# Performance work log

Measured on AMD Instinct MI355X. Metric: run time of the kernel, lower is better.

The kernel has to match this reference:

```python
import jax, jax.numpy as jnp
import numpy as np

B, N, T, E = 8, 512, 2048, 4096
D, TD, L = 768, 128, 4
V, TYPES = 30522, 64
MAX_NODE_LEN = 512


def setup_inputs() -> dict:
    key = jax.random.key(0)
    ks = jax.random.split(key, 12)
    tok_per_node = T // N  # 4 tokens per node
    node_types = jax.random.randint(ks[0], (B, N), 0, TYPES)
    node_token_ids = jax.random.randint(ks[1], (B, T), 0, V)
    token_seg_ids = jnp.tile(jnp.arange(T, dtype=jnp.int32) // tok_per_node, (B, 1))
    node_token_lens = jnp.full((B, N), tok_per_node, dtype=jnp.int32)
    graph_node_lens = jnp.full((B,), N, dtype=jnp.int32)
    edge_src = jax.random.randint(ks[2], (B, E), 0, N)
    edge_dst = jax.random.randint(ks[3], (B, E), 0, N)
    # edges_attrs used as PyG edge_weight (original passes LongTensor); cast to float
    edge_weight = jax.random.randint(ks[4], (B, E), 1, 4).astype(jnp.float32)
    s = 0.02
    type_table = jax.random.normal(ks[5], (TYPES, TD)) * s
    word_emb = jax.random.normal(ks[6], (V, D)) * s
    fusion_w = jax.random.normal(ks[7], (TD + D, D)) * s
    fusion_b = jnp.zeros((D,), jnp.float32)
    ggnn_w = jax.random.normal(ks[8], (L, D, D)) * s  # per-layer message weight
    gru_w_ih = jax.random.normal(ks[9], (3 * D, D)) * s  # [W_ir; W_iz; W_in]
    gru_w_hh = jax.random.normal(ks[10], (3 * D, D)) * s
    gru_b_ih = jnp.zeros((3 * D,), jnp.float32)
    gru_b_hh = jnp.zeros((3 * D,), jnp.float32)
    return dict(node_types=node_types, node_token_ids=node_token_ids,
                token_seg_ids=token_seg_ids, node_token_lens=node_token_lens,
                graph_node_lens=graph_node_lens, edge_src=edge_src,
                edge_dst=edge_dst, edge_weight=edge_weight,
                type_table=type_table, word_emb=word_emb,
                fusion_w=fusion_w, fusion_b=fusion_b, ggnn_w=ggnn_w,
                gru_w_ih=gru_w_ih, gru_w_hh=gru_w_hh,
                gru_b_ih=gru_b_ih, gru_b_hh=gru_b_hh)


def reference(node_types, node_token_ids, token_seg_ids, node_token_lens,
              graph_node_lens, edge_src, edge_dst, edge_weight,
              type_table, word_emb, fusion_w, fusion_b, ggnn_w,
              gru_w_ih, gru_w_hh, gru_b_ih, gru_b_hh):
    # --- embed lookups ---
    type_e = type_table[node_types]          # [B, N, TD]
    tok_e = word_emb[node_token_ids]         # [B, T, D]
    # --- ragged per-node token segment-mean ---
    seg_sum = jax.vmap(lambda d, s: jax.ops.segment_sum(d, s, num_segments=N))(
        tok_e, token_seg_ids)                # [B, N, D]
    text_e = seg_sum / node_token_lens[..., None].astype(seg_sum.dtype)
    # --- embed fusion ---
    fused = jnp.concatenate([type_e, text_e], axis=-1)  # [B, N, TD+D]
    h = jnp.einsum('bnf,fd->bnd', fused, fusion_w) + fusion_b  # [B, N, D]

    # --- GatedGraphConv: L rounds of (linear -> weighted scatter-add -> GRU) ---
    def scatter(m, src, dst, w):
        return jnp.zeros((N, m.shape[-1]), m.dtype).at[dst].add(m[src] * w[:, None])

    for l in range(L):
        m = jnp.einsum('bnd,de->bne', h, ggnn_w[l])
        agg = jax.vmap(scatter)(m, edge_src, edge_dst, edge_weight)  # [B, N, D]
        gi = agg @ gru_w_ih.T + gru_b_ih
        gh = h @ gru_w_hh.T + gru_b_hh
        ir, iz, in_ = jnp.split(gi, 3, axis=-1)
        hr, hz, hn = jnp.split(gh, 3, axis=-1)
        r = jax.nn.sigmoid(ir + hr)
        z = jax.nn.sigmoid(iz + hz)
        n = jnp.tanh(in_ + r * hn)
        h = (1.0 - z) * n + z * h

    # --- copy first min(node_lens, max_node_len) rows into zero-initialized res ---
    W = min(N, MAX_NODE_LEN)
    keep = jnp.minimum(graph_node_lens, MAX_NODE_LEN)           # [B]
    valid = jnp.arange(W)[None, :] < keep[:, None]              # [B, W]
    return jnp.where(valid[..., None], h[:, :W], 0.0)           # [B, W, D]
```

## Files before the change

kernel.cpp:

```cpp
#include <hip/hip_runtime.h>
#include <hip/hip_bf16.h>
#include <math.h>

namespace {
constexpr int B_  = 8;
constexpr int N_  = 512;
constexpr int T_  = 2048;
constexpr int E_  = 4096;
constexpr int D_  = 768;
constexpr int TD_ = 128;
constexpr int L_  = 4;
constexpr int F_  = TD_ + D_;
constexpr int G3_ = 3 * D_;
constexpr int BN  = B_ * N_;
constexpr int W_  = 512;
constexpr int TPN = T_ / N_;
}

typedef short bf16x8 __attribute__((ext_vector_type(8)));
typedef float f32x4  __attribute__((ext_vector_type(4)));

typedef const __attribute__((address_space(1))) void* gas1_cvp;
typedef __attribute__((address_space(3))) void*       as3_vp;

__device__ __forceinline__ unsigned short f2b(float f) {
    union { float f; unsigned u; } v; v.f = f;
    unsigned r = v.u + 0x7FFFu + ((v.u >> 16) & 1u);
    return (unsigned short)(r >> 16);
}
__device__ __forceinline__ float b2f(unsigned short u) {
    union { unsigned u; float f; } v; v.u = ((unsigned)u) << 16;
    return v.f;
}


__global__ void embed_fuse_kernel(const int* __restrict__ node_types,
                                  const int* __restrict__ tok_ids,
                                  const int* __restrict__ lens,
                                  const float* __restrict__ type_table,
                                  const float* __restrict__ word_emb,
                                  unsigned short* __restrict__ fused_bf)
{
    int i = blockIdx.x * blockDim.x + threadIdx.x;
    if (i >= BN * (F_ / 4)) return;
    int c4 = i % (F_ / 4);
    int bn = i / (F_ / 4);
    if (c4 < TD_ / 4) {
        int ty = node_types[bn];
        float4 v = *(const float4*)&type_table[(long long)ty * TD_ + c4 * 4];
        *(ushort4*)&fused_bf[(long long)bn * F_ + c4 * 4] =
            make_ushort4(f2b(v.x), f2b(v.y), f2b(v.z), f2b(v.w));
    } else {
        int d4 = c4 - TD_ / 4;
        int b  = bn / N_;
        int nn = bn % N_;
        float inv = 1.0f / (float)lens[bn];
        const int* tp = &tok_ids[b * T_ + nn * TPN];
        float sx = 0.f, sy = 0.f, sz = 0.f, sw = 0.f;
#pragma unroll
        for (int j = 0; j < TPN; ++j) {
            int tok = tp[j];
            float4 e = *(const float4*)&word_emb[(long long)tok * D_ + d4 * 4];
            sx += e.x; sy += e.y; sz += e.z; sw += e.w;
        }
        *(ushort4*)&fused_bf[(long long)bn * F_ + TD_ + d4 * 4] =
            make_ushort4(f2b(sx * inv), f2b(sy * inv), f2b(sz * inv), f2b(sw * inv));
    }
}

__global__ void adj_build_kernel(const int* __restrict__ esrc,
                                 const int* __restrict__ edst,
                                 const float* __restrict__ ew,
                                 float* __restrict__ adj)
{
    int i = blockIdx.x * blockDim.x + threadIdx.x;
    if (i >= B_ * E_) return;
    int b = i / E_;
    int s = esrc[i];
    int d = edst[i];
    atomicAdd(&adj[((long long)b * N_ + d) * N_ + s], ew[i]);
}


__global__ void cvt_f32_bf16(const float* __restrict__ s, unsigned short* __restrict__ d, int n4)
{
    int i = blockIdx.x * blockDim.x + threadIdx.x;
    if (i >= n4) return;
    float4 v = ((const float4*)s)[i];
    ((ushort4*)d)[i] = make_ushort4(f2b(v.x), f2b(v.y), f2b(v.z), f2b(v.w));
}

__global__ void cvt2_f32_bf16(const float* __restrict__ s0, unsigned short* __restrict__ d0,
                              const float* __restrict__ s1, unsigned short* __restrict__ d1,
                              int n4each)
{
    int i = blockIdx.x * blockDim.x + threadIdx.x;
    if (i < n4each) {
        float4 v = ((const float4*)s0)[i];
        ((ushort4*)d0)[i] = make_ushort4(f2b(v.x), f2b(v.y), f2b(v.z), f2b(v.w));
    } else if (i < 2 * n4each) {
        int j = i - n4each;
        float4 v = ((const float4*)s1)[j];
        ((ushort4*)d1)[j] = make_ushort4(f2b(v.x), f2b(v.y), f2b(v.z), f2b(v.w));
    }
}

__global__ void transpose_cvt(const float* __restrict__ s, unsigned short* __restrict__ d,
                              int R, int C)
{
    __shared__ float t[32][33];
    long long lo = (long long)blockIdx.z * R * C;
    s += lo; d += lo;
    int c0 = blockIdx.x * 32, r0 = blockIdx.y * 32;
    int tx = threadIdx.x, ty = threadIdx.y;
#pragma unroll
    for (int j = 0; j < 4; ++j)
        t[ty + j * 8][tx] = s[(long long)(r0 + ty + j * 8) * C + c0 + tx];
    __syncthreads();
#pragma unroll
    for (int j = 0; j < 4; ++j)
        d[(long long)(c0 + ty + j * 8) * R + r0 + tx] = f2b(t[tx][ty + j * 8]);
}


template <int MODE>
__device__ __forceinline__ void gemm_body(
    const unsigned short* __restrict__ A, const unsigned short* __restrict__ Bm,
    void* __restrict__ Cg, void* __restrict__ C2g, const float* __restrict__ bias,
    int M, int N, int K, long long zsC,
    short* __restrict__ As0, short* __restrict__ Bs0)
{
    const int tid  = threadIdx.x;
    const int lane = tid & 63;
    const int wv   = tid >> 6;
    const int wr   = wv >> 1, wc = wv & 1;
    const int row0 = blockIdx.y * 128;
    const int col0 = blockIdx.x * 128;

    f32x4 acc[4][4] = {};

    const int srow = lane >> 2;
    const int sk   = (lane & 3) * 8;
    const int fr   = lane & 15;
    const int kc   = (lane >> 4) * 8;

    auto stage = [&](int buf, int k0) {
        short* Ad = As0 + buf * (128 * 32);
        short* Bd = Bs0 + buf * (128 * 32);
#pragma unroll
        for (int r = 0; r < 2; ++r) {
            const unsigned short* ga = A + (long long)(row0 + r * 64 + wv * 16 + srow) * K + k0 + sk;
            __builtin_amdgcn_global_load_lds((gas1_cvp)ga,
                (as3_vp)(Ad + (r * 64 + wv * 16) * 32), 16, 0, 0);
            const unsigned short* gb = Bm + (long long)(col0 + r * 64 + wv * 16 + srow) * K + k0 + sk;
            __builtin_amdgcn_global_load_lds((gas1_cvp)gb,
                (as3_vp)(Bd + (r * 64 + wv * 16) * 32), 16, 0, 0);
        }
    };

    stage(0, 0);
    __syncthreads();

    const int nt = K >> 5;
    int cur = 0;
    for (int t = 0; t < nt; ++t) {
        if (t + 1 < nt) stage(cur ^ 1, (t + 1) << 5);
        const short* Ar = As0 + cur * (128 * 32);
        const short* Br = Bs0 + cur * (128 * 32);
        bf16x8 fa[4], fb[4];
#pragma unroll
        for (int m = 0; m < 4; ++m)
            fa[m] = *(const bf16x8*)&Ar[(wr * 64 + m * 16 + fr) * 32 + kc];
#pragma unroll
        for (int n = 0; n < 4; ++n)
            fb[n] = *(const bf16x8*)&Br[(wc * 64 + n * 16 + fr) * 32 + kc];
#pragma unroll
        for (int m = 0; m < 4; ++m)
#pragma unroll
            for (int n = 0; n < 4; ++n)
                acc[m][n] = __builtin_amdgcn_mfma_f32_16x16x32_bf16(fa[m], fb[n], acc[m][n], 0, 0, 0);
        __syncthreads();
        cur ^= 1;
    }

    const int fq = lane >> 4;
#pragma unroll
    for (int m = 0; m < 4; ++m) {
        const int gr = row0 + wr * 64 + m * 16 + fq * 4;
#pragma unroll
        for (int n = 0; n < 4; ++n) {
            const int gc = col0 + wc * 64 + n * 16 + fr;
            float v0 = acc[m][n][0], v1 = acc[m][n][1], v2 = acc[m][n][2], v3 = acc[m][n][3];
            if (bias != nullptr) {
                float bv = bias[gc];
                v0 += bv; v1 += bv; v2 += bv; v3 += bv;
            }
            if constexpr (MODE == 0 || MODE == 1) {
                float* C = (float*)Cg + zsC;
                C[(long long)(gr + 0) * N + gc] = v0;
                C[(long long)(gr + 1) * N + gc] = v1;
                C[(long long)(gr + 2) * N + gc] = v2;
                C[(long long)(gr + 3) * N + gc] = v3;
                if constexpr (MODE == 1) {
                    unsigned short* C2 = (unsigned short*)C2g;
                    C2[(long long)(gr + 0) * N + gc] = f2b(v0);
                    C2[(long long)(gr + 1) * N + gc] = f2b(v1);
                    C2[(long long)(gr + 2) * N + gc] = f2b(v2);
                    C2[(long long)(gr + 3) * N + gc] = f2b(v3);
                }
            } else if constexpr (MODE == 2) {
                unsigned short* C = (unsigned short*)Cg + zsC;
                C[(long long)(gr + 0) * N + gc] = f2b(v0);
                C[(long long)(gr + 1) * N + gc] = f2b(v1);
                C[(long long)(gr + 2) * N + gc] = f2b(v2);
                C[(long long)(gr + 3) * N + gc] = f2b(v3);
            } else {
                unsigned short* C = (unsigned short*)Cg;
                int b = gr >> 9;
                int s = gr & 511;
                ushort4 pk = make_ushort4(f2b(v0), f2b(v1), f2b(v2), f2b(v3));
                *(ushort4*)&C[((long long)b * N + gc) * 512 + s] = pk;
            }
        }
    }
}

template <int MODE>
__global__ __launch_bounds__(256)
void gemm_mfma(const unsigned short* __restrict__ Ag,
               const unsigned short* __restrict__ Bg,
               void* __restrict__ Cg, void* __restrict__ C2g,
               const float* __restrict__ bias,
               int M, int N, int K, long long sA, long long sB, long long sC)
{
    __shared__ __align__(16) short As[2 * 128 * 32];
    __shared__ __align__(16) short Bs[2 * 128 * 32];
    gemm_body<MODE>(Ag + blockIdx.z * sA, Bg + blockIdx.z * sB, Cg, C2g, bias,
                    M, N, K, blockIdx.z * sC, As, Bs);
}

template <int MODE>
__global__ __launch_bounds__(256)
void gemm_mfma_dual(const unsigned short* __restrict__ A0,
                    const unsigned short* __restrict__ A1,
                    const unsigned short* __restrict__ B0,
                    const unsigned short* __restrict__ B1,
                    void* __restrict__ C0, void* __restrict__ C1,
                    int M, int N, int K)
{
    __shared__ __align__(16) short As[2 * 128 * 32];
    __shared__ __align__(16) short Bs[2 * 128 * 32];
    const unsigned short* A  = blockIdx.z ? A1 : A0;
    const unsigned short* Bm = blockIdx.z ? B1 : B0;
    void* C = blockIdx.z ? C1 : C0;
    gemm_body<MODE>(A, Bm, C, nullptr, nullptr, M, N, K, 0, As, Bs);
}


__global__ void gru_kernel(const unsigned short* __restrict__ gi,
                           const unsigned short* __restrict__ gh,
                           const float* __restrict__ bih, const float* __restrict__ bhh,
                           float* __restrict__ h, unsigned short* __restrict__ hb,
                           const int* __restrict__ gl)
{
    int i = blockIdx.x * blockDim.x + threadIdx.x;
    if (i >= BN * (D_ / 4)) return;
    int d4 = i % (D_ / 4);
    int rn = i / (D_ / 4);
    int d = d4 * 4;
    const unsigned short* gir = gi + (long long)rn * G3_;
    const unsigned short* ghr = gh + (long long)rn * G3_;
    ushort4 uir = *(const ushort4*)&gir[d];
    ushort4 uiz = *(const ushort4*)&gir[D_ + d];
    ushort4 uin = *(const ushort4*)&gir[2 * D_ + d];
    ushort4 uhr = *(const ushort4*)&ghr[d];
    ushort4 uhz = *(const ushort4*)&ghr[D_ + d];
    ushort4 uhn = *(const ushort4*)&ghr[2 * D_ + d];
    float4 hv = *(const float4*)&h[(long long)rn * D_ + d];

    float a_ir[4] = {b2f(uir.x), b2f(uir.y), b2f(uir.z), b2f(uir.w)};
    float a_iz[4] = {b2f(uiz.x), b2f(uiz.y), b2f(uiz.z), b2f(uiz.w)};
    float a_in[4] = {b2f(uin.x), b2f(uin.y), b2f(uin.z), b2f(uin.w)};
    float a_hr[4] = {b2f(uhr.x), b2f(uhr.y), b2f(uhr.z), b2f(uhr.w)};
    float a_hz[4] = {b2f(uhz.x), b2f(uhz.y), b2f(uhz.z), b2f(uhz.w)};
    float a_hn[4] = {b2f(uhn.x), b2f(uhn.y), b2f(uhn.z), b2f(uhn.w)};
    float a_h[4]  = {hv.x, hv.y, hv.z, hv.w};
    float outv[4];
#pragma unroll
    for (int u = 0; u < 4; ++u) {
        float r = 1.f / (1.f + expf(-(a_ir[u] + bih[d + u] + a_hr[u] + bhh[d + u])));
        float z = 1.f / (1.f + expf(-(a_iz[u] + bih[D_ + d + u] + a_hz[u] + bhh[D_ + d + u])));
        float n = tanhf(a_in[u] + bih[2 * D_ + d + u] + r * (a_hn[u] + bhh[2 * D_ + d + u]));
        outv[u] = (1.f - z) * n + z * a_h[u];
    }
    if (gl != nullptr) {
        int b = rn / N_;
        int w = rn % N_;
        if (w >= min(gl[b], W_)) { outv[0] = outv[1] = outv[2] = outv[3] = 0.f; }
    }
    float4 o; o.x = outv[0]; o.y = outv[1]; o.z = outv[2]; o.w = outv[3];
    *(float4*)&h[(long long)rn * D_ + d] = o;
    *(ushort4*)&hb[(long long)rn * D_ + d] = make_ushort4(f2b(outv[0]), f2b(outv[1]),
                                                          f2b(outv[2]), f2b(outv[3]));
}


extern "C" void kernel_launch(void* const* d_in, const int* in_sizes, int n_in,
                              void* d_out, int out_size, void* d_ws, size_t ws_size,
                              hipStream_t stream)
{
    (void)in_sizes; (void)n_in; (void)out_size; (void)ws_size;

    const int*   node_types      = (const int*)d_in[0];
    const int*   node_token_ids  = (const int*)d_in[1];
    const int*   node_token_lens = (const int*)d_in[3];
    const int*   graph_node_lens = (const int*)d_in[4];
    const int*   edge_src        = (const int*)d_in[5];
    const int*   edge_dst        = (const int*)d_in[6];
    const float* edge_weight     = (const float*)d_in[7];
    const float* type_table      = (const float*)d_in[8];
    const float* word_emb        = (const float*)d_in[9];
    const float* fusion_w        = (const float*)d_in[10];
    const float* fusion_b        = (const float*)d_in[11];
    const float* ggnn_w          = (const float*)d_in[12];
    const float* gru_w_ih        = (const float*)d_in[13];
    const float* gru_w_hh        = (const float*)d_in[14];
    const float* gru_b_ih        = (const float*)d_in[15];
    const float* gru_b_hh        = (const float*)d_in[16];

    float* h = (float*)d_out;

    char* p = (char*)d_ws;
    auto carve = [&](size_t bytes) { char* r = p; p += (bytes + 255) & ~(size_t)255; return r; };

    unsigned short* gi_bf   = (unsigned short*)carve((size_t)BN * G3_ * 2);
    unsigned short* gh_bf   = (unsigned short*)carve((size_t)BN * G3_ * 2);
    unsigned short* h_bf    = (unsigned short*)carve((size_t)BN * D_ * 2);
    unsigned short* fused_bf= (unsigned short*)carve((size_t)BN * F_ * 2);
    float*          adj     = (float*)carve((size_t)B_ * N_ * N_ * 4);
    unsigned short* adj_bf  = (unsigned short*)carve((size_t)B_ * N_ * N_ * 2);
    unsigned short* mT      = (unsigned short*)carve((size_t)B_ * D_ * N_ * 2);
    unsigned short* agg_bf  = (unsigned short*)carve((size_t)BN * D_ * 2);
    unsigned short* fwT     = (unsigned short*)carve((size_t)D_ * F_ * 2);
    unsigned short* gwT     = (unsigned short*)carve((size_t)L_ * D_ * D_ * 2);
    unsigned short* wih_bf  = (unsigned short*)carve((size_t)G3_ * D_ * 2);
    unsigned short* whh_bf  = (unsigned short*)carve((size_t)G3_ * D_ * 2);

    hipMemsetAsync(adj, 0, (size_t)B_ * N_ * N_ * 4, stream);

    {   int n = BN * (F_ / 4);
        embed_fuse_kernel<<<(n + 255) / 256, 256, 0, stream>>>(
            node_types, node_token_ids, node_token_lens, type_table, word_emb, fused_bf); }
    {   int n = B_ * E_;
        adj_build_kernel<<<(n + 255) / 256, 256, 0, stream>>>(edge_src, edge_dst, edge_weight, adj); }

    cvt2_f32_bf16<<<(2 * G3_ * D_ / 4 + 255) / 256, 256, 0, stream>>>(
        gru_w_ih, wih_bf, gru_w_hh, whh_bf, G3_ * D_ / 4);
    cvt_f32_bf16<<<(B_ * N_ * N_ / 4 + 255) / 256, 256, 0, stream>>>(adj, adj_bf, B_ * N_ * N_ / 4);
    transpose_cvt<<<dim3(D_ / 32, F_ / 32, 1), dim3(32, 8), 0, stream>>>(fusion_w, fwT, F_, D_);
    transpose_cvt<<<dim3(D_ / 32, D_ / 32, L_), dim3(32, 8), 0, stream>>>(ggnn_w, gwT, D_, D_);

    dim3 blk(256);
    gemm_mfma<1><<<dim3(D_ / 128, BN / 128, 1), blk, 0, stream>>>(
        fused_bf, fwT, h, h_bf, fusion_b, BN, D_, F_, 0, 0, 0);

    for (int l = 0; l < L_; ++l) {
        gemm_mfma<3><<<dim3(D_ / 128, BN / 128, 1), blk, 0, stream>>>(
            h_bf, gwT + (size_t)l * D_ * D_, mT, nullptr, nullptr, BN, D_, D_, 0, 0, 0);
        gemm_mfma<2><<<dim3(D_ / 128, N_ / 128, B_), blk, 0, stream>>>(
            adj_bf, mT, agg_bf, nullptr, nullptr, N_, D_, N_,
            (long long)N_ * N_, (long long)D_ * N_, (long long)N_ * D_);
        gemm_mfma_dual<2><<<dim3(G3_ / 128, BN / 128, 2), blk, 0, stream>>>(
            agg_bf, h_bf, wih_bf, whh_bf, gi_bf, gh_bf, BN, G3_, D_);
        int n = BN * (D_ / 4);
        gru_kernel<<<(n + 255) / 256, 256, 0, stream>>>(
            gi_bf, gh_bf, gru_b_ih, gru_b_hh, h, h_bf,
            (l == L_ - 1) ? graph_node_lens : nullptr);
    }
}
```

Before: 642.2 us.

## Fold GGNN message weight into GRU input weights and reorder adjacency GEMM

Precomputes per-layer fused weights W_ih·W_g so the message GEMM is absorbed into the GRU input projection, then applies the adjacency GEMM to the 3D-wide projected result. This removes one GEMM launch and one intermediate per layer. In exchange the adjacency GEMM becomes three times wider and a one-off weight-product GEMM is added. It also introduces extra bf16 rounding of the fused weights.

Result: faster. 599.5 us (-6.6%).

```diff
diff --git a/kernel.cpp b/kernel.cpp
--- a/kernel.cpp
+++ b/kernel.cpp
@@ -90,18 +90,23 @@
     ((ushort4*)d)[i] = make_ushort4(f2b(v.x), f2b(v.y), f2b(v.z), f2b(v.w));
 }
 
-__global__ void cvt2_f32_bf16(const float* __restrict__ s0, unsigned short* __restrict__ d0,
-                              const float* __restrict__ s1, unsigned short* __restrict__ d1,
-                              int n4each)
-{
-    int i = blockIdx.x * blockDim.x + threadIdx.x;
-    if (i < n4each) {
+__global__ void cvt3_weights(const float* __restrict__ s0, unsigned short* __restrict__ d0,
+                             const float* __restrict__ s1, unsigned short* __restrict__ d1,
+                             const float* __restrict__ s2, unsigned short* __restrict__ d2,
+                             int n4a, int n4c)
+{
+    int i = blockIdx.x * blockDim.x + threadIdx.x;
+    if (i < n4a) {
         float4 v = ((const float4*)s0)[i];
         ((ushort4*)d0)[i] = make_ushort4(f2b(v.x), f2b(v.y), f2b(v.z), f2b(v.w));
-    } else if (i < 2 * n4each) {
-        int j = i - n4each;
+    } else if (i < 2 * n4a) {
+        int j = i - n4a;
         float4 v = ((const float4*)s1)[j];
         ((ushort4*)d1)[j] = make_ushort4(f2b(v.x), f2b(v.y), f2b(v.z), f2b(v.w));
+    } else if (i < 2 * n4a + n4c) {
+        int j = i - 2 * n4a;
+        float4 v = ((const float4*)s2)[j];
+        ((ushort4*)d2)[j] = make_ushort4(f2b(v.x), f2b(v.y), f2b(v.z), f2b(v.w));
     }
 }
 
@@ -109,8 +114,6 @@
                               int R, int C)
 {
     __shared__ float t[32][33];
-    long long lo = (long long)blockIdx.z * R * C;
-    s += lo; d += lo;
     int c0 = blockIdx.x * 32, r0 = blockIdx.y * 32;
     int tx = threadIdx.x, ty = threadIdx.y;
 #pragma unroll
@@ -239,21 +242,18 @@
                     M, N, K, blockIdx.z * sC, As, Bs);
 }
 
-template <int MODE>
 __global__ __launch_bounds__(256)
-void gemm_mfma_dual(const unsigned short* __restrict__ A0,
-                    const unsigned short* __restrict__ A1,
-                    const unsigned short* __restrict__ B0,
-                    const unsigned short* __restrict__ B1,
-                    void* __restrict__ C0, void* __restrict__ C1,
-                    int M, int N, int K)
+void gemm_qgh(const unsigned short* __restrict__ hbf,
+              const unsigned short* __restrict__ wfused_l,
+              const unsigned short* __restrict__ whh,
+              void* __restrict__ qT, void* __restrict__ gh)
 {
     __shared__ __align__(16) short As[2 * 128 * 32];
     __shared__ __align__(16) short Bs[2 * 128 * 32];
-    const unsigned short* A  = blockIdx.z ? A1 : A0;
-    const unsigned short* Bm = blockIdx.z ? B1 : B0;
-    void* C = blockIdx.z ? C1 : C0;
-    gemm_body<MODE>(A, Bm, C, nullptr, nullptr, M, N, K, 0, As, Bs);
+    if (blockIdx.z == 0)
+        gemm_body<3>(hbf, wfused_l, qT, nullptr, nullptr, BN, G3_, D_, 0, As, Bs);
+    else
+        gemm_body<2>(hbf, whh, gh, nullptr, nullptr, BN, G3_, D_, 0, As, Bs);
 }
 
 
@@ -335,16 +335,16 @@
 
     unsigned short* gi_bf   = (unsigned short*)carve((size_t)BN * G3_ * 2);
     unsigned short* gh_bf   = (unsigned short*)carve((size_t)BN * G3_ * 2);
+    unsigned short* qT      = (unsigned short*)carve((size_t)B_ * G3_ * N_ * 2);
     unsigned short* h_bf    = (unsigned short*)carve((size_t)BN * D_ * 2);
     unsigned short* fused_bf= (unsigned short*)carve((size_t)BN * F_ * 2);
     float*          adj     = (float*)carve((size_t)B_ * N_ * N_ * 4);
     unsigned short* adj_bf  = (unsigned short*)carve((size_t)B_ * N_ * N_ * 2);
-    unsigned short* mT      = (unsigned short*)carve((size_t)B_ * D_ * N_ * 2);
-    unsigned short* agg_bf  = (unsigned short*)carve((size_t)BN * D_ * 2);
     unsigned short* fwT     = (unsigned short*)carve((size_t)D_ * F_ * 2);
-    unsigned short* gwT     = (unsigned short*)carve((size_t)L_ * D_ * D_ * 2);
+    unsigned short* gwn_bf  = (unsigned short*)carve((size_t)L_ * D_ * D_ * 2);
     unsigned short* wih_bf  = (unsigned short*)carve((size_t)G3_ * D_ * 2);
     unsigned short* whh_bf  = (unsigned short*)carve((size_t)G3_ * D_ * 2);
+    unsigned short* wfused  = (unsigned short*)carve((size_t)L_ * G3_ * D_ * 2);
 
     hipMemsetAsync(adj, 0, (size_t)B_ * N_ * N_ * 4, stream);
 
@@ -354,24 +354,29 @@
     {   int n = B_ * E_;
         adj_build_kernel<<<(n + 255) / 256, 256, 0, stream>>>(edge_src, edge_dst, edge_weight, adj); }
 
-    cvt2_f32_bf16<<<(2 * G3_ * D_ / 4 + 255) / 256, 256, 0, stream>>>(
-        gru_w_ih, wih_bf, gru_w_hh, whh_bf, G3_ * D_ / 4);
+    {   int n4a = G3_ * D_ / 4;
+        int n4c = L_ * D_ * D_ / 4;
+        int tot = 2 * n4a + n4c;
+        cvt3_weights<<<(tot + 255) / 256, 256, 0, stream>>>(
+            gru_w_ih, wih_bf, gru_w_hh, whh_bf, ggnn_w, gwn_bf, n4a, n4c); }
     cvt_f32_bf16<<<(B_ * N_ * N_ / 4 + 255) / 256, 256, 0, stream>>>(adj, adj_bf, B_ * N_ * N_ / 4);
     transpose_cvt<<<dim3(D_ / 32, F_ / 32, 1), dim3(32, 8), 0, stream>>>(fusion_w, fwT, F_, D_);
-    transpose_cvt<<<dim3(D_ / 32, D_ / 32, L_), dim3(32, 8), 0, stream>>>(ggnn_w, gwT, D_, D_);
 
     dim3 blk(256);
+
+    gemm_mfma<2><<<dim3(D_ / 128, G3_ / 128, L_), blk, 0, stream>>>(
+        wih_bf, gwn_bf, wfused, nullptr, nullptr, G3_, D_, D_,
+        0, (long long)D_ * D_, (long long)G3_ * D_);
+
     gemm_mfma<1><<<dim3(D_ / 128, BN / 128, 1), blk, 0, stream>>>(
         fused_bf, fwT, h, h_bf, fusion_b, BN, D_, F_, 0, 0, 0);
 
     for (int l = 0; l < L_; ++l) {
-        gemm_mfma<3><<<dim3(D_ / 128, BN / 128, 1), blk, 0, stream>>>(
-            h_bf, gwT + (size_t)l * D_ * D_, mT, nullptr, nullptr, BN, D_, D_, 0, 0, 0);
-        gemm_mfma<2><<<dim3(D_ / 128, N_ / 128, B_), blk, 0, stream>>>(
-            adj_bf, mT, agg_bf, nullptr, nullptr, N_, D_, N_,
-            (long long)N_ * N_, (long long)D_ * N_, (long long)N_ * D_);
-        gemm_mfma_dual<2><<<dim3(G3_ / 128, BN / 128, 2), blk, 0, stream>>>(
-            agg_bf, h_bf, wih_bf, whh_bf, gi_bf, gh_bf, BN, G3_, D_);
+        gemm_qgh<<<dim3(G3_ / 128, BN / 128, 2), blk, 0, stream>>>(
+            h_bf, wfused + (size_t)l * G3_ * D_, whh_bf, qT, gh_bf);
+        gemm_mfma<2><<<dim3(G3_ / 128, N_ / 128, B_), blk, 0, stream>>>(
+            adj_bf, qT, gi_bf, nullptr, nullptr, N_, G3_, N_,
+            (long long)N_ * N_, (long long)G3_ * N_, (long long)N_ * G3_);
         int n = BN * (D_ / 4);
         gru_kernel<<<(n + 255) / 256, 256, 0, stream>>>(
             gi_bf, gh_bf, gru_b_ih, gru_b_hh, h, h_bf,
```
